# Kernel tuning notes

Hardware: AMD Instinct MI355X
Metric: run time of the kernel (lower is better)

The kernel has to match this reference:

```python
import jax, jax.numpy as jnp
import numpy as np

N_NODES = 50000
N_EDGES = 800000
N_FEAT = 128
HIDDEN = 256
BN_EPS = 1e-5


def setup_inputs() -> dict:
    key = jax.random.key(0)
    ks = jax.random.split(key, 8)
    x = jax.random.normal(ks[0], (N_NODES, N_FEAT), dtype=jnp.float32)
    edge_index = jax.random.randint(ks[1], (2, N_EDGES), 0, N_NODES, dtype=jnp.int64)
    # Xavier-uniform linear weights (as in weights_init), zero biases
    def xavier(k, fan_in, fan_out):
        lim = float(np.sqrt(6.0 / (fan_in + fan_out)))
        return jax.random.uniform(k, (fan_in, fan_out), jnp.float32, -lim, lim)
    return {
        "x": x,
        "edge_index": edge_index,
        "W1": xavier(ks[2], N_FEAT, HIDDEN),
        "b1": jnp.zeros((HIDDEN,), jnp.float32),
        "g1": jnp.ones((HIDDEN,), jnp.float32),
        "be1": jnp.zeros((HIDDEN,), jnp.float32),
        "W2": xavier(ks[3], HIDDEN, HIDDEN),
        "b2": jnp.zeros((HIDDEN,), jnp.float32),
        "g2": jnp.ones((HIDDEN,), jnp.float32),
        "be2": jnp.zeros((HIDDEN,), jnp.float32),
        "Wfc": xavier(ks[4], HIDDEN, HIDDEN),
        "bfc": jnp.zeros((HIDDEN,), jnp.float32),
    }


def gcn_conv(x, src, dst, deg_inv_sqrt, W, b):
    """PyG GCNConv: out_i = sum_{j->i} d_i^-1/2 d_j^-1/2 (x_j W) + b,
    with self-loops already appended to (src, dst)."""
    h = x @ W                                        # [N, out]
    norm = deg_inv_sqrt[src] * deg_inv_sqrt[dst]     # [E+N]
    msgs = h[src] * norm[:, None]                    # gather + scale
    out = jax.ops.segment_sum(msgs, dst, num_segments=x.shape[0])
    return out + b


def batch_norm(x, gamma, beta):
    # training-mode BatchNorm1d: batch stats over nodes, biased variance
    mean = jnp.mean(x, axis=0)
    var = jnp.mean(jnp.square(x - mean), axis=0)
    return (x - mean) * jax.lax.rsqrt(var + BN_EPS) * gamma + beta


def reference(x, edge_index, W1, b1, g1, be1, W2, b2, g2, be2, Wfc, bfc):
    n = x.shape[0]
    loop = jnp.arange(n, dtype=edge_index.dtype)
    src = jnp.concatenate([edge_index[0], loop])
    dst = jnp.concatenate([edge_index[1], loop])
    deg = jax.ops.segment_sum(jnp.ones_like(src, dtype=x.dtype), dst, num_segments=n)
    deg_inv_sqrt = jnp.where(deg > 0, jax.lax.rsqrt(jnp.maximum(deg, 1.0)), 0.0)

    h = gcn_conv(x, src, dst, deg_inv_sqrt, W1, b1)
    h = batch_norm(h, g1, be1)
    # dropout is identity in deterministic (eval) reference
    h = gcn_conv(h, src, dst, deg_inv_sqrt, W2, b2)
    h = batch_norm(h, g2, be2)
    return h @ Wfc + bfc
```

## Files before the change

kernel.cpp:

```cpp
#include <hip/hip_runtime.h>
#include <hip/hip_bf16.h>

#define NFEAT 128
#define HID 256
#define BN_EPS 1e-5f
#define NBIN 64

typedef __attribute__((ext_vector_type(8))) __bf16 bf16x8;
typedef __attribute__((ext_vector_type(4))) float f32x4;

static __device__ __forceinline__ float bflo(unsigned u) {
    union { unsigned x; float f; } c; c.x = u << 16; return c.f;
}
static __device__ __forceinline__ float bfhi(unsigned u) {
    union { unsigned x; float f; } c; c.x = u & 0xffff0000u; return c.f;
}

__global__ void k_count(const int* __restrict__ ei, int E, int* __restrict__ cnt,
                        int* __restrict__ rank) {
    int e = blockIdx.x * blockDim.x + threadIdx.x;
    if (e < E) rank[e] = atomicAdd(&cnt[ei[E + e]], 1);
}

__global__ void k_scan1(const int* __restrict__ cnt, int n, int* __restrict__ partial,
                        int* __restrict__ blk_total) {
    __shared__ int sh[256];
    int i = blockIdx.x * 256 + threadIdx.x;
    int v = (i < n) ? cnt[i] : 0;
    sh[threadIdx.x] = v;
    __syncthreads();
    for (int off = 1; off < 256; off <<= 1) {
        int x = (threadIdx.x >= off) ? sh[threadIdx.x - off] : 0;
        __syncthreads();
        sh[threadIdx.x] += x;
        __syncthreads();
    }
    if (i < n) partial[i] = sh[threadIdx.x] - v;
    if (threadIdx.x == 255) blk_total[blockIdx.x] = sh[255];
}

__global__ void k_scan2(int* __restrict__ blk, int nb) {
    __shared__ int sh[256];
    int t = threadIdx.x;
    int v = (t < nb) ? blk[t] : 0;
    sh[t] = v;
    __syncthreads();
    for (int off = 1; off < 256; off <<= 1) {
        int x = (t >= off) ? sh[t - off] : 0;
        __syncthreads();
        sh[t] += x;
        __syncthreads();
    }
    if (t < nb) blk[t] = sh[t] - v;
}

__global__ void k_finalize(const int* __restrict__ partial, const int* __restrict__ blk,
                           const int* __restrict__ cnt, int n, int* __restrict__ row_start,
                           float* __restrict__ dinv) {
    int i = blockIdx.x * blockDim.x + threadIdx.x;
    if (i < n) {
        row_start[i] = partial[i] + blk[i >> 8];
        dinv[i] = rsqrtf((float)(cnt[i] + 1));
    }
}

__global__ void k_fill(const int* __restrict__ ei, const int* __restrict__ rank,
                       const int* __restrict__ row_start, int E, int* __restrict__ col) {
    int e = blockIdx.x * blockDim.x + threadIdx.x;
    if (e < E) {
        int d = ei[E + e];
        col[row_start[d] + rank[e]] = ei[e];
    }
}

__global__ __launch_bounds__(256) void k_rvec(const int* __restrict__ rs,
                                              const int* __restrict__ rc,
                                              const int* __restrict__ col,
                                              const float* __restrict__ dinv,
                                              float* __restrict__ r, int N) {
    const int wid = blockIdx.x * 4 + (threadIdx.x >> 6);
    if (wid >= N) return;
    const int lane = threadIdx.x & 63;
    const int s = rs[wid];
    const int deg = rc[wid];
    float acc = 0.f;
    for (int e = lane; e < deg; e += 64) acc += dinv[col[s + e]];
#pragma unroll
    for (int m = 1; m < 64; m <<= 1) acc += __shfl_xor(acc, m);
    if (lane == 0) {
        float di = dinv[wid];
        r[wid] = di * (di + acc);
    }
}

__global__ void k_scale_cast(const float* __restrict__ in, const float* __restrict__ dinv,
                             __hip_bfloat16* __restrict__ out, int shift, int n4) {
    int i = blockIdx.x * blockDim.x + threadIdx.x;
    if (i < n4) {
        float d = dinv[i >> shift];
        float4 v = *(const float4*)(in + (size_t)i * 4);
        __hip_bfloat16* o = out + (size_t)i * 4;
        o[0] = __float2bfloat16(v.x * d);
        o[1] = __float2bfloat16(v.y * d);
        o[2] = __float2bfloat16(v.z * d);
        o[3] = __float2bfloat16(v.w * d);
    }
}

__global__ void k_transpose2(const float* __restrict__ W1, const float* __restrict__ Wf,
                             __hip_bfloat16* __restrict__ Wt1, __hip_bfloat16* __restrict__ Wtf) {
    int idx = blockIdx.x * 256 + threadIdx.x;
    if (idx < 32768) {
        int n = idx & 255;
        int k = idx >> 8;
        Wt1[n * 128 + k] = __float2bfloat16(W1[k * 256 + n]);
    } else {
        int base = idx - 32768;
        int n = base & 255;
        int k = base >> 8;
        Wtf[n * 256 + k] = __float2bfloat16(Wf[k * 256 + n]);
    }
}

__global__ void k_bnfold(const float* __restrict__ gs, const float* __restrict__ g,
                         const float* __restrict__ be, const float* __restrict__ b, float invN,
                         float* __restrict__ sc, float* __restrict__ bv) {
    int c = threadIdx.x;
    float s = 0.f, q = 0.f;
    for (int r = 0; r < NBIN; r++) {
        s += gs[r * 512 + c];
        q += gs[r * 512 + 256 + c];
    }
    float mean = s * invN;
    float var = q * invN - mean * mean;
    float scl = rsqrtf(var + BN_EPS) * g[c];
    float bb = b ? b[c] : 0.f;
    sc[c] = scl;
    bv[c] = (bb - mean) * scl + be[c];
}

__global__ __launch_bounds__(256) void k_foldW(const float* __restrict__ W1,
                                               const float* __restrict__ W2,
                                               const float* __restrict__ sc,
                                               __hip_bfloat16* __restrict__ WfT) {
    int k = blockIdx.x;
    int n = threadIdx.x;
    float acc = 0.f;
    for (int m = 0; m < 256; m++) acc += W1[k * 256 + m] * sc[m] * W2[m * 256 + n];
    WfT[(size_t)n * 128 + k] = __float2bfloat16(acc);
}

__global__ void k_uvec(const float* __restrict__ W2, const float* __restrict__ bv,
                       float* __restrict__ u) {
    int n = threadIdx.x;
    float acc = 0.f;
    for (int m = 0; m < 256; m++) acc += W2[m * 256 + n] * bv[m];
    u[n] = acc;
}

template <int PL>
static __device__ __forceinline__ void loadrow(const __hip_bfloat16* p, float* v) {
    if constexpr (PL == 4) {
        uint2 u = *(const uint2*)p;
        v[0] = bflo(u.x); v[1] = bfhi(u.x); v[2] = bflo(u.y); v[3] = bfhi(u.y);
    } else {
        unsigned u = *(const unsigned*)p;
        v[0] = bflo(u); v[1] = bfhi(u);
    }
}

template <int C>
__global__ __launch_bounds__(256) void k_spmm_w(const __hip_bfloat16* __restrict__ Hs,
                                                const int* __restrict__ rs,
                                                const int* __restrict__ rc,
                                                const int* __restrict__ col,
                                                const float* __restrict__ dinv,
                                                __hip_bfloat16* __restrict__ out,
                                                __hip_bfloat16* __restrict__ out2, int N) {
    constexpr int PL = C / 64;
    const int wid = blockIdx.x * 4 + (threadIdx.x >> 6);
    if (wid >= N) return;
    const int lane = threadIdx.x & 63;
    const int ch = lane * PL;
    const int s = rs[wid];
    const int deg = rc[wid];
    const float di = dinv[wid];

    float acc[PL];
    loadrow<PL>(Hs + (size_t)wid * C + ch, acc);

    int e = 0;
    for (; e + 8 <= deg; e += 8) {
        int idx[8];
#pragma unroll
        for (int j = 0; j < 8; j++) idx[j] = col[s + e + j];
        float v[8][PL];
#pragma unroll
        for (int j = 0; j < 8; j++) loadrow<PL>(Hs + (size_t)idx[j] * C + ch, v[j]);
#pragma unroll
        for (int j = 0; j < 8; j++)
#pragma unroll
            for (int i = 0; i < PL; i++) acc[i] += v[j][i];
    }
    for (; e < deg; e++) {
        int i0 = col[s + e];
        float v0[PL];
        loadrow<PL>(Hs + (size_t)i0 * C + ch, v0);
#pragma unroll
        for (int i = 0; i < PL; i++) acc[i] += v0[i];
    }
    union { unsigned u[PL / 2]; unsigned short us[PL]; } o;
#pragma unroll
    for (int i = 0; i < PL; i++) {
        __hip_bfloat16 b = __float2bfloat16(di * acc[i]);
        o.us[i] = *(unsigned short*)&b;
    }
    if constexpr (PL == 4)
        *(uint2*)(out + (size_t)wid * C + ch) = *(uint2*)o.u;
    else
        *(unsigned*)(out + (size_t)wid * C + ch) = o.u[0];
    if (out2) {
        union { unsigned u[PL / 2]; unsigned short us[PL]; } o2;
        float d2 = di * di;
#pragma unroll
        for (int i = 0; i < PL; i++) {
            __hip_bfloat16 b = __float2bfloat16(d2 * acc[i]);
            o2.us[i] = *(unsigned short*)&b;
        }
        if constexpr (PL == 4)
            *(uint2*)(out2 + (size_t)wid * C + ch) = *(uint2*)o2.u;
        else
            *(unsigned*)(out2 + (size_t)wid * C + ch) = o2.u[0];
    }
}

template <int K>
__global__ __launch_bounds__(256) void k_gemm2(const __hip_bfloat16* __restrict__ A,
                                               const __hip_bfloat16* __restrict__ Bt,
                                               const float* __restrict__ bias,
                                               __hip_bfloat16* __restrict__ outb,
                                               float* __restrict__ outf,
                                               float* __restrict__ gs,
                                               const float* __restrict__ rvec,
                                               const float* __restrict__ uvec,
                                               const float* __restrict__ bnsc,
                                               const float* __restrict__ bnof, int M) {
    constexpr int KS = K / 32;
    constexpr int LDR = K + 8;
    constexpr int ROWU4 = K / 8;
    __shared__ __align__(16) unsigned short Bs[128 * LDR];
    __shared__ float sred[4][128];
    __shared__ float qred[4][128];

    const int t = threadIdx.x;
    const int wv = t >> 6;
    const int lane = t & 63;
    const int mlane = lane & 15;
    const int quad = lane >> 4;
    const int m0 = blockIdx.x * 128;
    const int n0 = blockIdx.y * 128;

    bf16x8 a[2][KS];
#pragma unroll
    for (int mt = 0; mt < 2; mt++) {
        const int arow = m0 + wv * 32 + mt * 16 + mlane;
#pragma unroll
        for (int ks = 0; ks < KS; ks++) {
            bf16x8 raw = *(const bf16x8*)(A + (size_t)arow * K + ks * 32 + quad * 8);
            if (bnsc) {
                int cb = ks * 32 + quad * 8;
                union { bf16x8 v; unsigned u[4]; } cu; cu.v = raw;
                union { unsigned u[4]; unsigned short us[8]; } ou;
#pragma unroll
                for (int j = 0; j < 4; j++) {
                    float lo = bflo(cu.u[j]) * bnsc[cb + 2 * j] + bnof[cb + 2 * j];
                    float hi = bfhi(cu.u[j]) * bnsc[cb + 2 * j + 1] + bnof[cb + 2 * j + 1];
                    __hip_bfloat16 bl = __float2bfloat16(lo);
                    __hip_bfloat16 bh = __float2bfloat16(hi);
                    ou.us[2 * j] = *(unsigned short*)&bl;
                    ou.us[2 * j + 1] = *(unsigned short*)&bh;
                }
                a[mt][ks] = *(bf16x8*)ou.u;
            } else {
                a[mt][ks] = raw;
            }
        }
    }

#pragma unroll
    for (int i = 0; i < 128 * ROWU4 / 256; i++) {
        int idx = t + i * 256;
        int row = idx / ROWU4;
        int c = idx % ROWU4;
        uint4 v = *(const uint4*)(Bt + (size_t)(n0 + row) * K + c * 8);
        *(uint4*)(Bs + row * LDR + c * 8) = v;
    }
    __syncthreads();

    f32x4 acc[2][8];
#pragma unroll
    for (int mt = 0; mt < 2; mt++)
#pragma unroll
        for (int i = 0; i < 8; i++) acc[mt][i] = (f32x4){0.f, 0.f, 0.f, 0.f};

#pragma unroll
    for (int nt = 0; nt < 8; nt++) {
        const unsigned short* bp = Bs + (nt * 16 + mlane) * LDR + quad * 8;
#pragma unroll
        for (int ks = 0; ks < KS; ks++) {
            bf16x8 b = *(const bf16x8*)(bp + ks * 32);
            acc[0][nt] = __builtin_amdgcn_mfma_f32_16x16x32_bf16(a[0][ks], b, acc[0][nt], 0, 0, 0);
            acc[1][nt] = __builtin_amdgcn_mfma_f32_16x16x32_bf16(a[1][ks], b, acc[1][nt], 0, 0, 0);
        }
    }

    float rv[2][4] = {{0.f, 0.f, 0.f, 0.f}, {0.f, 0.f, 0.f, 0.f}};
    if (rvec) {
#pragma unroll
        for (int mt = 0; mt < 2; mt++)
#pragma unroll
            for (int r = 0; r < 4; r++) {
                int row = m0 + wv * 32 + mt * 16 + quad * 4 + r;
                if (row < M) rv[mt][r] = rvec[row];
            }
    }
    float sp[8], qp[8];
#pragma unroll
    for (int nt = 0; nt < 8; nt++) {
        int colx = n0 + nt * 16 + mlane;
        float bv = bias[colx];
        float uvn = uvec ? uvec[colx] : 0.f;
        float s = 0.f, q = 0.f;
#pragma unroll
        for (int mt = 0; mt < 2; mt++)
#pragma unroll
            for (int r = 0; r < 4; r++) {
                int row = m0 + wv * 32 + mt * 16 + quad * 4 + r;
                if (row < M) {
                    float h = acc[mt][nt][r] + bv + rv[mt][r] * uvn;
                    if (outb) outb[(size_t)row * HID + colx] = __float2bfloat16(h);
                    if (outf) outf[(size_t)row * HID + colx] = h;
                    s += h;
                    q += h * h;
                }
            }
        sp[nt] = s;
        qp[nt] = q;
    }
    if (gs) {
#pragma unroll
        for (int nt = 0; nt < 8; nt++) {
            sp[nt] += __shfl_xor(sp[nt], 16);
            sp[nt] += __shfl_xor(sp[nt], 32);
            qp[nt] += __shfl_xor(qp[nt], 16);
            qp[nt] += __shfl_xor(qp[nt], 32);
        }
        if (quad == 0) {
#pragma unroll
            for (int nt = 0; nt < 8; nt++) {
                sred[wv][nt * 16 + mlane] = sp[nt];
                qred[wv][nt * 16 + mlane] = qp[nt];
            }
        }
        __syncthreads();
        if (t < 128) {
            float ss = sred[0][t] + sred[1][t] + sred[2][t] + sred[3][t];
            float qq = qred[0][t] + qred[1][t] + qred[2][t] + qred[3][t];
            float* bin = gs + (blockIdx.x & (NBIN - 1)) * 512;
            atomicAdd(&bin[n0 + t], ss);
            atomicAdd(&bin[256 + n0 + t], qq);
        }
    }
}

extern "C" void kernel_launch(void* const* d_in, const int* in_sizes, int n_in, void* d_out,
                              int out_size, void* d_ws, size_t ws_size, hipStream_t stream) {
    const float* x = (const float*)d_in[0];
    const int* ei = (const int*)d_in[1];
    const float* W1 = (const float*)d_in[2];
    const float* b1 = (const float*)d_in[3];
    const float* g1 = (const float*)d_in[4];
    const float* be1 = (const float*)d_in[5];
    const float* W2 = (const float*)d_in[6];
    const float* b2 = (const float*)d_in[7];
    const float* g2 = (const float*)d_in[8];
    const float* be2 = (const float*)d_in[9];
    const float* Wfc = (const float*)d_in[10];
    const float* bfc = (const float*)d_in[11];
    float* out = (float*)d_out;

    const int N = in_sizes[0] / NFEAT;
    const int E = in_sizes[1] / 2;
    const float invN = 1.0f / (float)N;

    char* ws = (char*)d_ws;
    size_t off = 0;
    auto alloc = [&](size_t bytes) -> void* {
        void* p = ws + off;
        off += (bytes + 255) & ~(size_t)255;
        return p;
    };
    int* row_cnt = (int*)alloc((size_t)N * 4);
    int* partial = (int*)alloc((size_t)N * 4);
    int* row_start = (int*)alloc((size_t)N * 4);
    int* blk = (int*)alloc(256 * 4);
    float* dinv = (float*)alloc((size_t)N * 4);
    int* rank = (int*)alloc((size_t)E * 4);
    int* col_idx = (int*)alloc((size_t)E * 4);
    float* gs1 = (float*)alloc((size_t)NBIN * 512 * 4);
    float* gs2 = (float*)alloc((size_t)NBIN * 512 * 4);
    float* sc1 = (float*)alloc(256 * 4);
    float* bv1 = (float*)alloc(256 * 4);
    float* uvec = (float*)alloc(256 * 4);
    float* sc2 = (float*)alloc(256 * 4);
    float* of2 = (float*)alloc(256 * 4);
    float* rvec = (float*)alloc((size_t)(N + 128) * 4);
    __hip_bfloat16* Wt1 = (__hip_bfloat16*)alloc(256 * 128 * 2);
    __hip_bfloat16* Wtf = (__hip_bfloat16*)alloc(256 * 256 * 2);
    __hip_bfloat16* WfT = (__hip_bfloat16*)alloc(256 * 128 * 2);
    __hip_bfloat16* xs = (__hip_bfloat16*)alloc((size_t)(N + 128) * NFEAT * 2);
    __hip_bfloat16* aggX = (__hip_bfloat16*)alloc((size_t)(N + 128) * NFEAT * 2);
    __hip_bfloat16* t1s = (__hip_bfloat16*)alloc((size_t)(N + 128) * NFEAT * 2);
    __hip_bfloat16* h2 = (__hip_bfloat16*)alloc((size_t)(N + 128) * HID * 2);
    __hip_bfloat16* t2 = xs;

    hipMemsetAsync(row_cnt, 0, (size_t)N * 4, stream);
    hipMemsetAsync(gs1, 0, (size_t)NBIN * 512 * 4 * 2, stream);

    k_count<<<(E + 255) / 256, 256, 0, stream>>>(ei, E, row_cnt, rank);
    int nblk = (N + 255) / 256;
    k_scan1<<<nblk, 256, 0, stream>>>(row_cnt, N, partial, blk);
    k_scan2<<<1, 256, 0, stream>>>(blk, nblk);
    k_finalize<<<nblk, 256, 0, stream>>>(partial, blk, row_cnt, N, row_start, dinv);
    k_fill<<<(E + 255) / 256, 256, 0, stream>>>(ei, rank, row_start, E, col_idx);

    k_transpose2<<<384, 256, 0, stream>>>(W1, Wfc, Wt1, Wtf);

    k_scale_cast<<<(N * NFEAT / 4 + 255) / 256, 256, 0, stream>>>(x, dinv, xs, 5, N * NFEAT / 4);

    int sg = (N + 3) / 4;
    k_rvec<<<sg, 256, 0, stream>>>(row_start, row_cnt, col_idx, dinv, rvec, N);

    dim3 gg((N + 127) / 128, 2);
    k_spmm_w<NFEAT><<<sg, 256, 0, stream>>>(xs, row_start, row_cnt, col_idx, dinv, aggX, t1s, N);
    k_gemm2<NFEAT><<<gg, 256, 0, stream>>>(aggX, Wt1, b1, nullptr, nullptr, gs1,
                                           nullptr, nullptr, nullptr, nullptr, N);
    k_bnfold<<<1, 256, 0, stream>>>(gs1, g1, be1, b1, invN, sc1, bv1);
    k_foldW<<<128, 256, 0, stream>>>(W1, W2, sc1, WfT);
    k_uvec<<<1, 256, 0, stream>>>(W2, bv1, uvec);
    k_spmm_w<NFEAT><<<sg, 256, 0, stream>>>(t1s, row_start, row_cnt, col_idx, dinv, t2, nullptr, N);
    k_gemm2<NFEAT><<<gg, 256, 0, stream>>>(t2, WfT, b2, h2, nullptr, gs2,
                                           rvec, uvec, nullptr, nullptr, N);
    k_bnfold<<<1, 256, 0, stream>>>(gs2, g2, be2, nullptr, invN, sc2, of2);
    k_gemm2<HID><<<gg, 256, 0, stream>>>(h2, Wtf, bfc, nullptr, out, nullptr,
                                         nullptr, nullptr, sc2, of2, N);
}
```

Measured before the change: 376.2 us.

## Double-buffer K-chunks in GEMM with smaller shared tile for higher occupancy

The GEMM kernel now splits K into 64-wide chunks. It double-buffers the B tile in shared memory and prefetches the next A fragments while the current chunk runs MFMAs. Shared memory use drops, especially for the K=256 GEMM, and launch bounds request 4 blocks per CU, so occupancy should rise and load latency overlap with compute. The stats reduction reuses the B buffer and is now selected by a template flag, which needs an extra barrier and adds per-chunk syncs.

```diff
diff --git a/kernel.cpp b/kernel.cpp
--- a/kernel.cpp
+++ b/kernel.cpp
@@ -234,23 +234,22 @@
     }
 }
 
-template <int K>
-__global__ __launch_bounds__(256) void k_gemm2(const __hip_bfloat16* __restrict__ A,
-                                               const __hip_bfloat16* __restrict__ Bt,
-                                               const float* __restrict__ bias,
-                                               __hip_bfloat16* __restrict__ outb,
-                                               float* __restrict__ outf,
-                                               float* __restrict__ gs,
-                                               const float* __restrict__ rvec,
-                                               const float* __restrict__ uvec,
-                                               const float* __restrict__ bnsc,
-                                               const float* __restrict__ bnof, int M) {
-    constexpr int KS = K / 32;
-    constexpr int LDR = K + 8;
-    constexpr int ROWU4 = K / 8;
-    __shared__ __align__(16) unsigned short Bs[128 * LDR];
-    __shared__ float sred[4][128];
-    __shared__ float qred[4][128];
+template <int K, bool STATS>
+__global__ __launch_bounds__(256, 4) void k_gemm2(const __hip_bfloat16* __restrict__ A,
+                                                  const __hip_bfloat16* __restrict__ Bt,
+                                                  const float* __restrict__ bias,
+                                                  __hip_bfloat16* __restrict__ outb,
+                                                  float* __restrict__ outf,
+                                                  float* __restrict__ gs,
+                                                  const float* __restrict__ rvec,
+                                                  const float* __restrict__ uvec,
+                                                  const float* __restrict__ bnsc,
+                                                  const float* __restrict__ bnof, int M) {
+    constexpr int NC = K / 64;
+    constexpr int LDR = 72;
+    __shared__ __align__(16) unsigned short Bs[2 * 128 * LDR];
+    float* sred = (float*)Bs;
+    float* qred = sred + 512;
 
     const int t = threadIdx.x;
     const int wv = t >> 6;
@@ -259,43 +258,43 @@
     const int quad = lane >> 4;
     const int m0 = blockIdx.x * 128;
     const int n0 = blockIdx.y * 128;
-
-    bf16x8 a[2][KS];
-#pragma unroll
-    for (int mt = 0; mt < 2; mt++) {
-        const int arow = m0 + wv * 32 + mt * 16 + mlane;
-#pragma unroll
-        for (int ks = 0; ks < KS; ks++) {
-            bf16x8 raw = *(const bf16x8*)(A + (size_t)arow * K + ks * 32 + quad * 8);
-            if (bnsc) {
-                int cb = ks * 32 + quad * 8;
-                union { bf16x8 v; unsigned u[4]; } cu; cu.v = raw;
-                union { unsigned u[4]; unsigned short us[8]; } ou;
-#pragma unroll
-                for (int j = 0; j < 4; j++) {
-                    float lo = bflo(cu.u[j]) * bnsc[cb + 2 * j] + bnof[cb + 2 * j];
-                    float hi = bfhi(cu.u[j]) * bnsc[cb + 2 * j + 1] + bnof[cb + 2 * j + 1];
-                    __hip_bfloat16 bl = __float2bfloat16(lo);
-                    __hip_bfloat16 bh = __float2bfloat16(hi);
-                    ou.us[2 * j] = *(unsigned short*)&bl;
-                    ou.us[2 * j + 1] = *(unsigned short*)&bh;
+    const int arow0 = m0 + wv * 32 + mlane;
+
+    auto stage = [&](int c, int buf) {
+#pragma unroll
+        for (int i = 0; i < 4; i++) {
+            int idx = t + i * 256;
+            int row = idx >> 3;
+            int c4 = idx & 7;
+            uint4 v = *(const uint4*)(Bt + (size_t)(n0 + row) * K + c * 64 + c4 * 8);
+            *(uint4*)(Bs + buf * (128 * LDR) + row * LDR + c4 * 8) = v;
+        }
+    };
+    auto loadA = [&](int c, bf16x8 (&dst)[2][2]) {
+#pragma unroll
+        for (int mt = 0; mt < 2; mt++)
+#pragma unroll
+            for (int ks = 0; ks < 2; ks++) {
+                int cb = c * 64 + ks * 32 + quad * 8;
+                bf16x8 raw = *(const bf16x8*)(A + (size_t)(arow0 + mt * 16) * K + cb);
+                if (bnsc) {
+                    union { bf16x8 v; unsigned u[4]; } cu; cu.v = raw;
+                    union { unsigned u[4]; unsigned short us[8]; } ou;
+#pragma unroll
+                    for (int j = 0; j < 4; j++) {
+                        float lo = bflo(cu.u[j]) * bnsc[cb + 2 * j] + bnof[cb + 2 * j];
+                        float hi = bfhi(cu.u[j]) * bnsc[cb + 2 * j + 1] + bnof[cb + 2 * j + 1];
+                        __hip_bfloat16 bl = __float2bfloat16(lo);
+                        __hip_bfloat16 bh = __float2bfloat16(hi);
+                        ou.us[2 * j] = *(unsigned short*)&bl;
+                        ou.us[2 * j + 1] = *(unsigned short*)&bh;
+                    }
+                    dst[mt][ks] = *(bf16x8*)ou.u;
+                } else {
+                    dst[mt][ks] = raw;
                 }
-                a[mt][ks] = *(bf16x8*)ou.u;
-            } else {
-                a[mt][ks] = raw;
             }
-        }
-    }
-
-#pragma unroll
-    for (int i = 0; i < 128 * ROWU4 / 256; i++) {
-        int idx = t + i * 256;
-        int row = idx / ROWU4;
-        int c = idx % ROWU4;
-        uint4 v = *(const uint4*)(Bt + (size_t)(n0 + row) * K + c * 8);
-        *(uint4*)(Bs + row * LDR + c * 8) = v;
-    }
-    __syncthreads();
+    };
 
     f32x4 acc[2][8];
 #pragma unroll
@@ -303,15 +302,32 @@
 #pragma unroll
         for (int i = 0; i < 8; i++) acc[mt][i] = (f32x4){0.f, 0.f, 0.f, 0.f};
 
-#pragma unroll
-    for (int nt = 0; nt < 8; nt++) {
-        const unsigned short* bp = Bs + (nt * 16 + mlane) * LDR + quad * 8;
-#pragma unroll
-        for (int ks = 0; ks < KS; ks++) {
-            bf16x8 b = *(const bf16x8*)(bp + ks * 32);
-            acc[0][nt] = __builtin_amdgcn_mfma_f32_16x16x32_bf16(a[0][ks], b, acc[0][nt], 0, 0, 0);
-            acc[1][nt] = __builtin_amdgcn_mfma_f32_16x16x32_bf16(a[1][ks], b, acc[1][nt], 0, 0, 0);
-        }
+    bf16x8 aP[2][2], aQ[2][2];
+    loadA(0, aP);
+    stage(0, 0);
+
+    auto mmachunk = [&](int c, bf16x8 (&ac)[2][2]) {
+        const unsigned short* base = Bs + (c & 1) * (128 * LDR);
+#pragma unroll
+        for (int nt = 0; nt < 8; nt++) {
+            const unsigned short* bp = base + (nt * 16 + mlane) * LDR + quad * 8;
+#pragma unroll
+            for (int ks = 0; ks < 2; ks++) {
+                bf16x8 b = *(const bf16x8*)(bp + ks * 32);
+                acc[0][nt] = __builtin_amdgcn_mfma_f32_16x16x32_bf16(ac[0][ks], b, acc[0][nt], 0, 0, 0);
+                acc[1][nt] = __builtin_amdgcn_mfma_f32_16x16x32_bf16(ac[1][ks], b, acc[1][nt], 0, 0, 0);
+            }
+        }
+    };
+
+#pragma unroll
+    for (int c = 0; c < NC; c++) {
+        __syncthreads();
+        if (c + 1 < NC) {
+            stage(c + 1, (c + 1) & 1);
+            if ((c & 1) == 0) loadA(c + 1, aQ); else loadA(c + 1, aP);
+        }
+        if ((c & 1) == 0) mmachunk(c, aP); else mmachunk(c, aQ);
     }
 
     float rv[2][4] = {{0.f, 0.f, 0.f, 0.f}, {0.f, 0.f, 0.f, 0.f}};
@@ -347,7 +363,7 @@
         sp[nt] = s;
         qp[nt] = q;
     }
-    if (gs) {
+    if constexpr (STATS) {
 #pragma unroll
         for (int nt = 0; nt < 8; nt++) {
             sp[nt] += __shfl_xor(sp[nt], 16);
@@ -355,17 +371,18 @@
             qp[nt] += __shfl_xor(qp[nt], 16);
             qp[nt] += __shfl_xor(qp[nt], 32);
         }
+        __syncthreads();
         if (quad == 0) {
 #pragma unroll
             for (int nt = 0; nt < 8; nt++) {
-                sred[wv][nt * 16 + mlane] = sp[nt];
-                qred[wv][nt * 16 + mlane] = qp[nt];
+                sred[wv * 128 + nt * 16 + mlane] = sp[nt];
+                qred[wv * 128 + nt * 16 + mlane] = qp[nt];
             }
         }
         __syncthreads();
         if (t < 128) {
-            float ss = sred[0][t] + sred[1][t] + sred[2][t] + sred[3][t];
-            float qq = qred[0][t] + qred[1][t] + qred[2][t] + qred[3][t];
+            float ss = sred[t] + sred[128 + t] + sred[256 + t] + sred[384 + t];
+            float qq = qred[t] + qred[128 + t] + qred[256 + t] + qred[384 + t];
             float* bin = gs + (blockIdx.x & (NBIN - 1)) * 512;
             atomicAdd(&bin[n0 + t], ss);
             atomicAdd(&bin[256 + n0 + t], qq);
@@ -443,15 +460,15 @@
 
     dim3 gg((N + 127) / 128, 2);
     k_spmm_w<NFEAT><<<sg, 256, 0, stream>>>(xs, row_start, row_cnt, col_idx, dinv, aggX, t1s, N);
-    k_gemm2<NFEAT><<<gg, 256, 0, stream>>>(aggX, Wt1, b1, nullptr, nullptr, gs1,
-                                           nullptr, nullptr, nullptr, nullptr, N);
+    k_gemm2<NFEAT, true><<<gg, 256, 0, stream>>>(aggX, Wt1, b1, nullptr, nullptr, gs1,
+                                                 nullptr, nullptr, nullptr, nullptr, N);
     k_bnfold<<<1, 256, 0, stream>>>(gs1, g1, be1, b1, invN, sc1, bv1);
     k_foldW<<<128, 256, 0, stream>>>(W1, W2, sc1, WfT);
     k_uvec<<<1, 256, 0, stream>>>(W2, bv1, uvec);
     k_spmm_w<NFEAT><<<sg, 256, 0, stream>>>(t1s, row_start, row_cnt, col_idx, dinv, t2, nullptr, N);
-    k_gemm2<NFEAT><<<gg, 256, 0, stream>>>(t2, WfT, b2, h2, nullptr, gs2,
-                                           rvec, uvec, nullptr, nullptr, N);
+    k_gemm2<NFEAT, true><<<gg, 256, 0, stream>>>(t2, WfT, b2, h2, nullptr, gs2,
+                                                 rvec, uvec, nullptr, nullptr, N);
     k_bnfold<<<1, 256, 0, stream>>>(gs2, g2, be2, nullptr, invN, sc2, of2);
-    k_gemm2<HID><<<gg, 256, 0, stream>>>(h2, Wtf, bfc, nullptr, out, nullptr,
-                                         nullptr, nullptr, sc2, of2, N);
-}
+    k_gemm2<HID, false><<<gg, 256, 0, stream>>>(h2, Wtf, bfc, nullptr, out, nullptr,
+                                                nullptr, nullptr, sc2, of2, N);
+}
```

Measured after the change: 347.6 us. -7.6%, faster.
